# Optimization experiments

Hardware: AMD Instinct MI355X
Metric: run time of the kernel (lower is better)

Reference implementation:

```python
import jax, jax.numpy as jnp
import numpy as np

HEADS = 4

def _dwconv(x, w, pad):
    # depthwise conv, NCHW, kernel [C,1,k,k]
    return jax.lax.conv_general_dilated(
        x, w, window_strides=(1, 1), padding=((pad, pad), (pad, pad)),
        feature_group_count=x.shape[1],
        dimension_numbers=('NCHW', 'OIHW', 'NCHW'))

def _l2norm(t):
    # matches torch F.normalize(dim=-1, eps=1e-12)
    n = jnp.sqrt(jnp.sum(t * t, axis=-1, keepdims=True))
    return t / jnp.maximum(n, 1e-12)

def _reshape_attn(q, k, v, temp, if_box):
    b, c, hw0 = q.shape
    factor = HEADS
    ch = c // HEADS
    pad = (-hw0) % factor

    def prep(t):
        t = jnp.pad(t, ((0, 0), (0, 0), (0, pad)))
        hw = t.shape[-1] // factor
        if if_box:  # 'b (head c) (factor hw) -> b head (c factor) hw'
            t = t.reshape(b, HEADS, ch, factor, hw)
        else:       # 'b (head c) (hw factor) -> b head (c factor) hw'
            t = t.reshape(b, HEADS, ch, hw, factor).transpose(0, 1, 2, 4, 3)
        return t.reshape(b, HEADS, ch * factor, hw)

    qq, kk, vv = prep(q), prep(k), prep(v)
    qq, kk = _l2norm(qq), _l2norm(kk)
    attn = jnp.einsum('bhdn,bhen->bhde', qq, kk) * temp  # temp [heads,1,1]
    e = jnp.exp(attn)
    attn = e / (jnp.sum(e, axis=-1, keepdims=True) + 1.0)  # softmax_1
    o = jnp.einsum('bhde,bhen->bhdn', attn, vv)
    hw = o.shape[-1]
    if if_box:
        o = o.reshape(b, HEADS, ch, factor, hw).reshape(b, c, factor * hw)
    else:
        o = o.reshape(b, HEADS, ch, factor, hw).transpose(0, 1, 2, 4, 3).reshape(b, c, hw * factor)
    return o[:, :, :hw0]

def _conv1x1(x, w):
    return jnp.einsum('bchw,oc->bohw', x, w)

def _forward(x, temperature, w_qkv, w_dw3, w_dw5, w_dw7, w_fuse, b_fuse, w_proj):
    b, c, h, w = x.shape
    ch = c // 2
    # sort first half of channels along h then w
    xh = x[:, :ch]
    idx_h = jnp.argsort(xh, axis=-2)
    xs = jnp.take_along_axis(xh, idx_h, axis=-2)
    idx_w = jnp.argsort(xs, axis=-1)
    xs = jnp.take_along_axis(xs, idx_w, axis=-1)
    x = jnp.concatenate([xs, x[:, ch:]], axis=1)

    q = _conv1x1(x, w_qkv)  # [b,5c,h,w]
    cat = jnp.concatenate([_dwconv(q, w_dw3, 1), _dwconv(q, w_dw5, 2), _dwconv(q, w_dw7, 3)], axis=1)
    qkv = _conv1x1(cat, w_fuse) + b_fuse[None, :, None, None]
    q1, k1, q2, k2, v = jnp.split(qkv, 5, axis=1)

    hw = h * w
    vf = v.reshape(b, c, hw)
    idx = jnp.argsort(vf, axis=-1)
    vs = jnp.take_along_axis(vf, idx, axis=-1)
    gat = lambda t: jnp.take_along_axis(t.reshape(b, c, hw), idx, axis=-1)

    out1 = _reshape_attn(gat(q1), gat(k1), vs, temperature, True)
    out2 = _reshape_attn(gat(q2), gat(k2), vs, temperature, False)

    inv = jnp.argsort(idx, axis=-1)  # scatter(out, 2, idx, out) == unsort
    out1 = jnp.take_along_axis(out1, inv, axis=-1).reshape(b, c, h, w)
    out2 = jnp.take_along_axis(out2, inv, axis=-1).reshape(b, c, h, w)

    out = _conv1x1(out1 * out2, w_proj)
    r = out[:, :ch]
    r = jnp.take_along_axis(r, jnp.argsort(idx_w, axis=-1), axis=-1)
    r = jnp.take_along_axis(r, jnp.argsort(idx_h, axis=-2), axis=-2)
    return jnp.concatenate([r, out[:, ch:]], axis=1)

def setup_inputs() -> dict:
    key = jax.random.key(0)
    ks = jax.random.split(key, 8)
    b, c, h, w = 2, 64, 192, 192
    x = jax.random.normal(ks[0], (b, c, h, w), jnp.float32)
    temperature = jnp.ones((HEADS, 1, 1), jnp.float32)
    w_qkv = jax.random.normal(ks[1], (5 * c, c), jnp.float32) * 0.05
    w_dw3 = jax.random.normal(ks[2], (5 * c, 1, 3, 3), jnp.float32) * 0.1
    w_dw5 = jax.random.normal(ks[3], (5 * c, 1, 5, 5), jnp.float32) * 0.05
    w_dw7 = jax.random.normal(ks[4], (5 * c, 1, 7, 7), jnp.float32) * 0.03
    w_fuse = jax.random.normal(ks[5], (5 * c, 15 * c), jnp.float32) * 0.02
    b_fuse = jnp.zeros((5 * c,), jnp.float32)
    w_proj = jax.random.normal(ks[6], (c, c), jnp.float32) * 0.05
    return {'x': x, 'temperature': temperature, 'w_qkv': w_qkv, 'w_dw3': w_dw3,
            'w_dw5': w_dw5, 'w_dw7': w_dw7, 'w_fuse': w_fuse, 'b_fuse': b_fuse,
            'w_proj': w_proj}

def reference(x, temperature, w_qkv, w_dw3, w_dw5, w_dw7, w_fuse, b_fuse, w_proj):
    return _forward(x, temperature, w_qkv, w_dw3, w_dw5, w_dw7, w_fuse, b_fuse, w_proj)
```

## Files before the change

kernel.cpp:

```cpp
#include <hip/hip_runtime.h>
#include <stdint.h>
#include <stddef.h>

constexpr int IMH = 192;
constexpr int IMW = 192;
constexpr int HW  = 36864;
constexpr int BB  = 2;
constexpr int CC  = 64;
constexpr int CHF = 32;
constexpr int C5  = 320;
constexpr int NQ  = 9216;
constexpr int CROWS = 64;
constexpr int CHWN  = CROWS * IMW;
constexpr int NCHUNK = 32;
constexpr int CHN = HW / 4 / NCHUNK;
constexpr int NSEG = 16;
constexpr int SEGN = HW / NSEG;
constexpr int NBIN = 2048;

typedef float fx4 __attribute__((ext_vector_type(4)));
typedef _Float16 f16;
typedef _Float16 f16x8 __attribute__((ext_vector_type(8)));
typedef float f32x4 __attribute__((ext_vector_type(4)));

static __device__ __forceinline__ uint32_t f2s(float f) {
    uint32_t u = __float_as_uint(f);
    return (u & 0x80000000u) ? ~u : (u | 0x80000000u);
}
static __device__ __forceinline__ float s2f(uint32_t s) {
    uint32_t u = (s & 0x80000000u) ? (s & 0x7FFFFFFFu) : ~s;
    return __uint_as_float(u);
}

static __device__ void bitonic256(uint64_t* keys, int tid) {
    for (unsigned k = 2; k <= 256; k <<= 1) {
        for (unsigned j = k >> 1; j; j >>= 1) {
            __syncthreads();
            unsigned i = ((tid & ~(j - 1)) << 1) | (tid & (j - 1));
            unsigned p = i | j;
            bool up = ((i & k) == 0);
            uint64_t a = keys[i], b = keys[p];
            if ((a > b) == up) { keys[i] = b; keys[p] = a; }
        }
    }
    __syncthreads();
}

__global__ void k_copy_back(const float* __restrict__ x, float* __restrict__ A) {
    int i = blockIdx.x * 256 + threadIdx.x;
    int b = i / (CHF * HW);
    int r = i % (CHF * HW);
    size_t o = ((size_t)(b * CC) + CHF) * HW + r;
    A[o] = x[o];
}

__global__ __launch_bounds__(128) void k_sort_h(const float* __restrict__ x, float* __restrict__ A,
                                                int* __restrict__ idx_h) {
    __shared__ uint64_t keys[256];
    int tid = threadIdx.x;
    int blk = blockIdx.x;
    int w = blk % IMW;
    int c = (blk / IMW) % CHF;
    int b = blk / (IMW * CHF);
    const float* col = x + ((size_t)(b * CC) + c) * HW + w;
    for (int i = tid; i < 256; i += 128)
        keys[i] = (i < IMH) ? ((((uint64_t)f2s(col[(size_t)i * IMW])) << 32) | (uint32_t)i) : ~0ull;
    bitonic256(keys, tid);
    float* ocol = A + ((size_t)(b * CC) + c) * HW + w;
    int* icol = idx_h + ((size_t)(b * CHF) + c) * HW + w;
    for (int i = tid; i < IMH; i += 128) {
        uint64_t k = keys[i];
        ocol[(size_t)i * IMW] = s2f((uint32_t)(k >> 32));
        icol[(size_t)i * IMW] = (int)(k & 0xFFFFFFFFull);
    }
}

__global__ __launch_bounds__(128) void k_sort_w(float* __restrict__ A, int* __restrict__ idx_w) {
    __shared__ uint64_t keys[256];
    int tid = threadIdx.x;
    int blk = blockIdx.x;
    int h = blk % IMH;
    int c = (blk / IMH) % CHF;
    int b = blk / (IMH * CHF);
    float* row = A + ((size_t)(b * CC) + c) * HW + (size_t)h * IMW;
    for (int i = tid; i < 256; i += 128)
        keys[i] = (i < IMW) ? ((((uint64_t)f2s(row[i])) << 32) | (uint32_t)i) : ~0ull;
    bitonic256(keys, tid);
    int* irow = idx_w + ((size_t)(b * CHF) + c) * HW + (size_t)h * IMW;
    for (int i = tid; i < IMW; i += 128) {
        uint64_t k = keys[i];
        row[i] = s2f((uint32_t)(k >> 32));
        irow[i] = (int)(k & 0xFFFFFFFFull);
    }
}

__global__ __launch_bounds__(256) void k_gemm_q(const float* __restrict__ wq, const float* __restrict__ A,
                                                float* __restrict__ q) {
    __shared__ float Wt[64][68];
    __shared__ float Xt[64][68];
    int tid = threadIdx.x;
    int n0 = blockIdx.x * 64, m0 = blockIdx.y * 64, b = blockIdx.z;
    for (int l = 0; l < 16; ++l) {
        int idx = l * 256 + tid;
        int cc = idx & 63, m = idx >> 6;
        Wt[cc][m] = wq[(size_t)(m0 + m) * 64 + cc];
    }
    for (int l = 0; l < 16; ++l) {
        int idx = l * 256 + tid;
        int n = idx & 63, cc = idx >> 6;
        Xt[cc][n] = A[((size_t)(b * CC) + cc) * HW + n0 + n];
    }
    __syncthreads();
    int ty = tid >> 4, tx = tid & 15;
    float acc[4][4] = {};
    for (int cc = 0; cc < 64; ++cc) {
        float4 av = *(const float4*)&Wt[cc][ty * 4];
        float4 bv = *(const float4*)&Xt[cc][tx * 4];
        float aa[4] = {av.x, av.y, av.z, av.w};
        float bb[4] = {bv.x, bv.y, bv.z, bv.w};
        #pragma unroll
        for (int i = 0; i < 4; ++i)
            #pragma unroll
            for (int j = 0; j < 4; ++j)
                acc[i][j] = fmaf(aa[i], bb[j], acc[i][j]);
    }
    for (int i = 0; i < 4; ++i) {
        float4 o;
        o.x = acc[i][0]; o.y = acc[i][1]; o.z = acc[i][2]; o.w = acc[i][3];
        *(float4*)&q[((size_t)(b * C5) + m0 + ty * 4 + i) * HW + n0 + tx * 4] = o;
    }
}

template <int KS>
__global__ __launch_bounds__(256) void k_dwconv(const float* __restrict__ q, const float* __restrict__ wd,
                                                float* __restrict__ slice, int r0) {
    constexpr int PAD = KS / 2;
    constexpr int EXT = 32 + 2 * PAD;
    __shared__ float tile[EXT][EXT];
    int tid = threadIdx.x;
    int b = blockIdx.z, c = blockIdx.y;
    int t = blockIdx.x;
    int ty0 = r0 + (t / 6) * 32, tx0 = (t % 6) * 32;
    const float* src = q + ((size_t)(b * C5) + c) * HW;
    for (int i = tid; i < EXT * EXT; i += 256) {
        int iy = i / EXT, ix = i % EXT;
        int gy = ty0 + iy - PAD, gx = tx0 + ix - PAD;
        float v = 0.f;
        if (gy >= 0 && gy < IMH && gx >= 0 && gx < IMW) v = src[gy * IMW + gx];
        tile[iy][ix] = v;
    }
    __syncthreads();
    float wreg[KS * KS];
    #pragma unroll
    for (int i = 0; i < KS * KS; ++i) wreg[i] = wd[(size_t)c * KS * KS + i];
    float* dst = slice + ((size_t)(b * C5) + c) * CHWN;
    #pragma unroll
    for (int k = 0; k < 4; ++k) {
        int pix = k * 256 + tid;
        int py = pix >> 5, px = pix & 31;
        float acc = 0.f;
        #pragma unroll
        for (int ky = 0; ky < KS; ++ky)
            #pragma unroll
            for (int kx = 0; kx < KS; ++kx)
                acc = fmaf(tile[py + ky][px + kx], wreg[ky * KS + kx], acc);
        dst[(ty0 - r0 + py) * IMW + tx0 + px] = acc;
    }
}

__global__ __launch_bounds__(256) void k_gemm_fuse(const float* __restrict__ wf,
                                                   const float* __restrict__ slice, const float* __restrict__ bias,
                                                   float* __restrict__ qkv, int g, int r0) {
    __shared__ f16 Ah[64][40];
    __shared__ f16 Al[64][40];
    int tid = threadIdx.x;
    int n0 = blockIdx.x * 128, m0 = blockIdx.y * 64, b = blockIdx.z;
    int lane = tid & 63, wv = tid >> 6;
    int l15 = lane & 15, lg = lane >> 4;
    int nwave = n0 + wv * 32;
    int sm = tid >> 2, skr = (tid & 3) * 8;
    int gk = g * 320;
    f32x4 acc[4][2];
    #pragma unroll
    for (int i = 0; i < 4; ++i)
        #pragma unroll
        for (int j = 0; j < 2; ++j)
            acc[i][j] = (f32x4){0.f, 0.f, 0.f, 0.f};

    const float* xcol = slice + (size_t)(b * C5) * CHWN + nwave + l15;
    const float* wrow = wf + (size_t)(m0 + sm) * 960 + gk + skr;

    for (int k0 = 0; k0 < 320; k0 += 32) {
        if (k0) __syncthreads();
        {
            float4 w0 = *(const float4*)(wrow + k0);
            float4 w1 = *(const float4*)(wrow + k0 + 4);
            float wvv[8] = {w0.x, w0.y, w0.z, w0.w, w1.x, w1.y, w1.z, w1.w};
            f16x8 hv, lv;
            #pragma unroll
            for (int j = 0; j < 8; ++j) {
                f16 h = (f16)wvv[j];
                hv[j] = h;
                lv[j] = (f16)(wvv[j] - (float)h);
            }
            *(f16x8*)&Ah[sm][skr] = hv;
            *(f16x8*)&Al[sm][skr] = lv;
        }
        float xv[2][8];
        #pragma unroll
        for (int fn = 0; fn < 2; ++fn)
            #pragma unroll
            for (int j = 0; j < 8; ++j)
                xv[fn][j] = xcol[(size_t)(k0 + lg * 8 + j) * CHWN + fn * 16];
        __syncthreads();
        f16x8 bh[2], bl[2];
        #pragma unroll
        for (int fn = 0; fn < 2; ++fn)
            #pragma unroll
            for (int j = 0; j < 8; ++j) {
                float v = xv[fn][j];
                f16 h = (f16)v;
                bh[fn][j] = h;
                bl[fn][j] = (f16)(v - (float)h);
            }
        #pragma unroll
        for (int fm = 0; fm < 4; ++fm) {
            f16x8 ah = *(const f16x8*)&Ah[fm * 16 + l15][lg * 8];
            f16x8 al = *(const f16x8*)&Al[fm * 16 + l15][lg * 8];
            #pragma unroll
            for (int fn = 0; fn < 2; ++fn) {
                acc[fm][fn] = __builtin_amdgcn_mfma_f32_16x16x32_f16(ah, bh[fn], acc[fm][fn], 0, 0, 0);
                acc[fm][fn] = __builtin_amdgcn_mfma_f32_16x16x32_f16(ah, bl[fn], acc[fm][fn], 0, 0, 0);
                acc[fm][fn] = __builtin_amdgcn_mfma_f32_16x16x32_f16(al, bh[fn], acc[fm][fn], 0, 0, 0);
            }
        }
    }

    #pragma unroll
    for (int fm = 0; fm < 4; ++fm) {
        #pragma unroll
        for (int r = 0; r < 4; ++r) {
            int m = m0 + fm * 16 + lg * 4 + r;
            size_t base = ((size_t)(b * C5) + m) * HW + (size_t)r0 * IMW;
            if (g == 0) {
                float bv = bias[m];
                #pragma unroll
                for (int fn = 0; fn < 2; ++fn)
                    qkv[base + nwave + fn * 16 + l15] = acc[fm][fn][r] + bv;
            } else {
                #pragma unroll
                for (int fn = 0; fn < 2; ++fn)
                    qkv[base + nwave + fn * 16 + l15] += acc[fm][fn][r];
            }
        }
    }
}

__global__ void k_build_keys(const float* __restrict__ qkv, uint64_t* __restrict__ keyA) {
    int j = blockIdx.x * 256 + threadIdx.x;
    int row = blockIdx.y;
    int b = row >> 6, c = row & 63;
    float v = qkv[((size_t)(b * C5) + 256 + c) * HW + j];
    keyA[(size_t)row * HW + j] = (((uint64_t)f2s(v)) << 32) | (uint32_t)j;
}

__global__ __launch_bounds__(256) void k_rcount(const uint64_t* __restrict__ in, uint32_t* __restrict__ cntG,
                                                int shift) {
    __shared__ uint32_t hist[NBIN];
    int t = threadIdx.x;
    int seg = blockIdx.x, row = blockIdx.y;
    #pragma unroll
    for (int k = 0; k < NBIN / 256; ++k) hist[k * 256 + t] = 0;
    __syncthreads();
    const uint64_t* src = in + (size_t)row * HW + (size_t)seg * SEGN;
    #pragma unroll
    for (int i = 0; i < SEGN / 256; ++i) {
        unsigned d = (unsigned)(src[i * 256 + t] >> shift) & (NBIN - 1);
        atomicAdd(&hist[d], 1u);
    }
    __syncthreads();
    uint32_t* dstc = cntG + ((size_t)row * NSEG + seg) * NBIN;
    #pragma unroll
    for (int k = 0; k < NBIN / 256; ++k) dstc[k * 256 + t] = hist[k * 256 + t];
}

__global__ __launch_bounds__(256) void k_rscan(uint32_t* __restrict__ cntG) {
    __shared__ uint32_t tot[NBIN];
    __shared__ uint32_t gsum[256];
    __shared__ uint32_t gbase[256];
    int t = threadIdx.x;
    int row = blockIdx.x;
    uint32_t* base = cntG + (size_t)row * NSEG * NBIN;
    uint32_t loc = 0;
    #pragma unroll
    for (int k = 0; k < NBIN / 256; ++k) {
        int bn = t * (NBIN / 256) + k;
        uint32_t s = 0;
        for (int sg = 0; sg < NSEG; ++sg) s += base[sg * NBIN + bn];
        tot[bn] = s;
        loc += s;
    }
    gsum[t] = loc;
    __syncthreads();
    if (t == 0) {
        uint32_t acc = 0;
        for (int i = 0; i < 256; ++i) { uint32_t v = gsum[i]; gbase[i] = acc; acc += v; }
    }
    __syncthreads();
    uint32_t run = gbase[t];
    #pragma unroll
    for (int k = 0; k < NBIN / 256; ++k) {
        int bn = t * (NBIN / 256) + k;
        uint32_t tv = tot[bn];
        uint32_t r2 = run;
        for (int sg = 0; sg < NSEG; ++sg) {
            uint32_t cv = base[sg * NBIN + bn];
            base[sg * NBIN + bn] = r2;
            r2 += cv;
        }
        run += tv;
    }
}

__global__ __launch_bounds__(256) void k_rscatter(const uint64_t* __restrict__ in, uint64_t* __restrict__ out,
                                                  const uint32_t* __restrict__ cntG, int shift) {
    __shared__ uint16_t wcnt[4][NBIN];
    __shared__ uint32_t runbase[NBIN];
    int t = threadIdx.x;
    int w = t >> 6, lane = t & 63;
    int seg = blockIdx.x, row = blockIdx.y;
    const uint32_t* cbase = cntG + ((size_t)row * NSEG + seg) * NBIN;
    #pragma unroll
    for (int k = 0; k < NBIN / 256; ++k) runbase[k * 256 + t] = cbase[k * 256 + t];
    const uint64_t* src = in + (size_t)row * HW + (size_t)seg * SEGN;
    uint64_t* dst = out + (size_t)row * HW;
    for (int i = 0; i < SEGN / 256; ++i) {
        __syncthreads();
        #pragma unroll
        for (int k = 0; k < NBIN / 256; ++k)
            ((uint64_t*)wcnt)[k * 256 + t] = 0;
        __syncthreads();
        uint64_t kv = src[i * 256 + t];
        unsigned d = (unsigned)(kv >> shift) & (NBIN - 1);
        uint64_t peers = ~0ull;
        #pragma unroll
        for (int bit = 0; bit < 11; ++bit) {
            uint64_t bm = __ballot((d >> bit) & 1u);
            peers &= ((d >> bit) & 1u) ? bm : ~bm;
        }
        unsigned lanerank = (unsigned)__popcll(peers & ((1ull << lane) - 1ull));
        unsigned wtotal = (unsigned)__popcll(peers);
        if (lanerank == 0) wcnt[w][d] = (uint16_t)wtotal;
        __syncthreads();
        unsigned wpre = 0;
        #pragma unroll
        for (int ww = 0; ww < 4; ++ww) {
            unsigned cv = wcnt[ww][d];
            if (ww < w) wpre += cv;
        }
        unsigned pos = runbase[d] + wpre + lanerank;
        dst[pos] = kv;
        __syncthreads();
        #pragma unroll
        for (int k = 0; k < NBIN / 256; ++k) {
            int bn = k * 256 + t;
            runbase[bn] += (uint32_t)wcnt[0][bn] + wcnt[1][bn] + wcnt[2][bn] + wcnt[3][bn];
        }
    }
}

__global__ void k_unpack(const uint64_t* __restrict__ keys, float* __restrict__ vs, int* __restrict__ idxv) {
    int j = blockIdx.x * 256 + threadIdx.x;
    int row = blockIdx.y;
    size_t o = (size_t)row * HW + j;
    uint64_t k = keys[o];
    vs[o] = s2f((uint32_t)(k >> 32));
    idxv[o] = (int)(k & 0xFFFFFFFFull);
}

__global__ __launch_bounds__(1024) void k_gather4(const int* __restrict__ idxv, const float* __restrict__ qkv,
                                                  float* __restrict__ g4) {
    int i = blockIdx.x;
    int row = (i & 7) * 16 + ((i >> 3) & 15);
    int jh = i >> 7;
    int b = row >> 6, cg = row & 63;
    const int* irow = idxv + (size_t)row * HW + jh * (HW / 2);
    size_t S4 = (size_t)BB * CC * HW;
    int tid = threadIdx.x;
    for (int ph = 0; ph < 4; ++ph) {
        const float* src = qkv + ((size_t)(b * C5) + ph * 64 + cg) * HW;
        float* dst = g4 + (size_t)ph * S4 + (size_t)row * HW + jh * (HW / 2);
        #pragma unroll 2
        for (int j = tid; j < HW / 2; j += 1024)
            dst[j] = src[irow[j]];
        __syncthreads();
    }
}

__global__ __launch_bounds__(256) void k_attn_qk(const float* __restrict__ g4,
                                                 float* __restrict__ partS, float* __restrict__ partN) {
    __shared__ float Qs[16][68];
    __shared__ float Ks[16][68];
    __shared__ float nqs[4][64];
    __shared__ float nks[4][64];
    int tid = threadIdx.x;
    int ychunk = blockIdx.x;
    int z = blockIdx.y;
    int vi = z & 1, hh = (z >> 1) & 3, b = z >> 3;
    size_t S4 = (size_t)BB * CC * HW;
    const float* Q = g4 + (vi ? 2 * S4 : (size_t)0);
    const float* Kp = g4 + (vi ? 3 * S4 : S4);
    int ty = tid >> 4, tx = tid & 15;
    float acc[4][4] = {};
    float nq = 0.f, nk = 0.f;
    int d0 = tid & 63, kset = tid >> 6;
    int nbase0 = ychunk * CHN;
    for (int it = 0; it < CHN / 16; ++it) {
        int nb0 = nbase0 + it * 16;
        __syncthreads();
        #pragma unroll
        for (int l = 0; l < 4; ++l) {
            int idx = l * 256 + tid;
            int d = idx >> 4, kk = idx & 15;
            int n = nb0 + kk;
            int cch = hh * 16 + (d >> 2), f = d & 3;
            size_t off = ((size_t)(b * CC) + cch) * HW + (vi ? (size_t)(n * 4 + f) : (size_t)(f * NQ + n));
            Qs[kk][d] = Q[off];
            Ks[kk][d] = Kp[off];
        }
        __syncthreads();
        #pragma unroll
        for (int kk = 0; kk < 16; ++kk) {
            float4 av = *(const float4*)&Qs[kk][ty * 4];
            float4 bv = *(const float4*)&Ks[kk][tx * 4];
            float aa[4] = {av.x, av.y, av.z, av.w};
            float bb[4] = {bv.x, bv.y, bv.z, bv.w};
            #pragma unroll
            for (int i = 0; i < 4; ++i)
                #pragma unroll
                for (int j = 0; j < 4; ++j)
                    acc[i][j] = fmaf(aa[i], bb[j], acc[i][j]);
        }
        #pragma unroll
        for (int kk2 = 0; kk2 < 4; ++kk2) {
            float qv = Qs[kset * 4 + kk2][d0];
            float kv = Ks[kset * 4 + kk2][d0];
            nq = fmaf(qv, qv, nq);
            nk = fmaf(kv, kv, nk);
        }
    }
    size_t sb = ((size_t)z * NCHUNK + ychunk) * 4096;
    #pragma unroll
    for (int i = 0; i < 4; ++i)
        #pragma unroll
        for (int j = 0; j < 4; ++j)
            partS[sb + (size_t)(ty * 4 + i) * 64 + tx * 4 + j] = acc[i][j];
    nqs[kset][d0] = nq;
    nks[kset][d0] = nk;
    __syncthreads();
    if (tid < 64) {
        float sq = nqs[0][tid] + nqs[1][tid] + nqs[2][tid] + nqs[3][tid];
        float sk = nks[0][tid] + nks[1][tid] + nks[2][tid] + nks[3][tid];
        size_t nb2 = ((size_t)z * NCHUNK + ychunk) * 128;
        partN[nb2 + tid] = sq;
        partN[nb2 + 64 + tid] = sk;
    }
}

__global__ __launch_bounds__(256) void k_attn_softmax(const float* __restrict__ partS,
                                                      const float* __restrict__ partN,
                                                      const float* __restrict__ temp, float* __restrict__ attnT) {
    __shared__ float nqv[64], nkv[64];
    __shared__ float pbuf[64][65];
    __shared__ float rred[64][4];
    __shared__ float rsum[64];
    int tid = threadIdx.x;
    int z = blockIdx.x;
    int hh = (z >> 1) & 3;
    if (tid < 128) {
        float s = 0.f;
        for (int ch = 0; ch < NCHUNK; ++ch) s += partN[((size_t)z * NCHUNK + ch) * 128 + tid];
        float nv = fmaxf(sqrtf(s), 1e-12f);
        if (tid < 64) nqv[tid] = nv; else nkv[tid - 64] = nv;
    }
    __syncthreads();
    float tf = temp[hh];
    int d = tid >> 2, qq = tid & 3;
    float psum = 0.f;
    for (int e = qq * 16; e < qq * 16 + 16; ++e) {
        float s = 0.f;
        for (int ch = 0; ch < NCHUNK; ++ch) s += partS[((size_t)z * NCHUNK + ch) * 4096 + (size_t)d * 64 + e];
        float p = expf(tf * s / (nqv[d] * nkv[e]));
        pbuf[d][e] = p;
        psum += p;
    }
    rred[d][qq] = psum;
    __syncthreads();
    if (tid < 64) rsum[tid] = rred[tid][0] + rred[tid][1] + rred[tid][2] + rred[tid][3] + 1.0f;
    __syncthreads();
    for (int e = qq * 16; e < qq * 16 + 16; ++e)
        attnT[(size_t)z * 4096 + (size_t)e * 64 + d] = pbuf[d][e] / rsum[d];
}

__global__ __launch_bounds__(256) void k_attn_av(const float* __restrict__ attnT, const float* __restrict__ vs,
                                                 float* __restrict__ O1, float* __restrict__ O2) {
    __shared__ float at_s[4096];
    int tid = threadIdx.x;
    int z = blockIdx.y;
    int vi = z & 1, hh = (z >> 1) & 3, b = z >> 3;
    for (int l = 0; l < 16; ++l) at_s[l * 256 + tid] = attnT[(size_t)z * 4096 + l * 256 + tid];
    __syncthreads();
    int n = blockIdx.x * 256 + tid;
    float acc[64];
    #pragma unroll
    for (int d = 0; d < 64; ++d) acc[d] = 0.f;
    for (int e = 0; e < 64; ++e) {
        int cch = hh * 16 + (e >> 2), f = e & 3;
        size_t p = vi ? (size_t)(n * 4 + f) : (size_t)(f * NQ + n);
        float vv = vs[((size_t)(b * CC) + cch) * HW + p];
        const float* ar = &at_s[e * 64];
        #pragma unroll
        for (int d4 = 0; d4 < 16; ++d4) {
            float4 a4 = *(const float4*)&ar[d4 * 4];
            acc[d4 * 4 + 0] = fmaf(a4.x, vv, acc[d4 * 4 + 0]);
            acc[d4 * 4 + 1] = fmaf(a4.y, vv, acc[d4 * 4 + 1]);
            acc[d4 * 4 + 2] = fmaf(a4.z, vv, acc[d4 * 4 + 2]);
            acc[d4 * 4 + 3] = fmaf(a4.w, vv, acc[d4 * 4 + 3]);
        }
    }
    float* Ob = vi ? O2 : O1;
    #pragma unroll
    for (int d = 0; d < 64; ++d) {
        int cch = hh * 16 + (d >> 2), f = d & 3;
        size_t p = vi ? (size_t)(n * 4 + f) : (size_t)(f * NQ + n);
        Ob[((size_t)(b * CC) + cch) * HW + p] = acc[d];
    }
}

__global__ void k_prod_scatter(const float* __restrict__ O1, const float* __restrict__ O2,
                               const int* __restrict__ idxv, float* __restrict__ pu) {
    int j = blockIdx.x * 256 + threadIdx.x;
    int row = blockIdx.y;
    size_t o = (size_t)row * HW + j;
    int p = idxv[o];
    pu[(size_t)row * HW + p] = O1[o] * O2[o];
}

__global__ __launch_bounds__(256) void k_gemm_proj(const float* __restrict__ wp, const float* __restrict__ pu,
                                                   float* __restrict__ op) {
    __shared__ float wt[4096];
    int tid = threadIdx.x;
    for (int l = 0; l < 16; ++l) {
        int i = l * 256 + tid;
        int m = i >> 6, c = i & 63;
        wt[c * 64 + m] = wp[i];
    }
    __syncthreads();
    int b = blockIdx.y;
    int n = blockIdx.x * 256 + tid;
    float acc[64];
    #pragma unroll
    for (int m = 0; m < 64; ++m) acc[m] = 0.f;
    const float* src = pu + (size_t)(b * CC) * HW + n;
    for (int c = 0; c < 64; ++c) {
        float xv = src[(size_t)c * HW];
        const float* wr = &wt[c * 64];
        #pragma unroll
        for (int m4 = 0; m4 < 16; ++m4) {
            float4 w4 = *(const float4*)&wr[m4 * 4];
            acc[m4 * 4 + 0] = fmaf(w4.x, xv, acc[m4 * 4 + 0]);
            acc[m4 * 4 + 1] = fmaf(w4.y, xv, acc[m4 * 4 + 1]);
            acc[m4 * 4 + 2] = fmaf(w4.z, xv, acc[m4 * 4 + 2]);
            acc[m4 * 4 + 3] = fmaf(w4.w, xv, acc[m4 * 4 + 3]);
        }
    }
    float* dst = op + (size_t)(b * CC) * HW + n;
    for (int m = 0; m < 64; ++m) dst[(size_t)m * HW] = acc[m];
}

__global__ void k_final(const float* __restrict__ op, const int* __restrict__ idx_h,
                        const int* __restrict__ idx_w, float* __restrict__ out) {
    int i = blockIdx.x * 256 + threadIdx.x;
    int p = i % HW;
    int c = (i / HW) % CC;
    int b = i / (HW * CC);
    float v = op[i];
    if (c < CHF) {
        int h = p / IMW, w = p % IMW;
        size_t ib = ((size_t)(b * CHF) + c) * HW;
        int W0 = idx_w[ib + h * IMW + w];
        int H0 = idx_h[ib + h * IMW + W0];
        out[((size_t)(b * CC) + c) * HW + H0 * IMW + W0] = v;
    } else {
        out[i] = v;
    }
}

extern "C" void kernel_launch(void* const* d_in, const int* in_sizes, int n_in,
                              void* d_out, int out_size, void* d_ws, size_t ws_size,
                              hipStream_t stream) {
    (void)in_sizes; (void)n_in; (void)out_size; (void)ws_size;
    const float* x    = (const float*)d_in[0];
    const float* temp = (const float*)d_in[1];
    const float* wq   = (const float*)d_in[2];
    const float* wd3  = (const float*)d_in[3];
    const float* wd5  = (const float*)d_in[4];
    const float* wd7  = (const float*)d_in[5];
    const float* wf   = (const float*)d_in[6];
    const float* bf   = (const float*)d_in[7];
    const float* wp   = (const float*)d_in[8];
    float* out = (float*)d_out;
    float* ws = (float*)d_ws;

    int*      idx_h = (int*)(ws + 0);
    int*      idx_w = (int*)(ws + 2359296);
    float*    A     = ws + 4718592;
    float*    slice = ws + 4718592;
    float*    q     = ws + 12582912;
    float*    qkv   = ws + 36175872;
    uint64_t* keyA  = (uint64_t*)(ws + 12582912);
    uint64_t* keyB  = (uint64_t*)(ws + 22020096);
    float*    vs    = ws + 31457280;
    uint32_t* cntG  = (uint32_t*)(ws + 4718592);
    int*      idxv  = (int*)(ws + 4718592);
    float*    g4    = ws + 12582912;
    float*    O1    = ws + 36175872;
    float*    O2    = ws + 40894464;
    float*    pu    = ws + 45613056;
    float*    op    = ws + 50331648;
    float*    partS = ws + 55050240;
    float*    partN = ws + 57147392;
    float*    attnT = ws + 57212928;

    k_copy_back<<<9216, 256, 0, stream>>>(x, A);
    k_sort_h<<<12288, 128, 0, stream>>>(x, A, idx_h);
    k_sort_w<<<12288, 128, 0, stream>>>(A, idx_w);
    k_gemm_q<<<dim3(576, 5, 2), 256, 0, stream>>>(wq, A, q);

    for (int g = 0; g < 3; ++g) {
        for (int chunk = 0; chunk < 3; ++chunk) {
            int r0 = chunk * CROWS;
            if (g == 0)      k_dwconv<3><<<dim3(12, 320, 2), 256, 0, stream>>>(q, wd3, slice, r0);
            else if (g == 1) k_dwconv<5><<<dim3(12, 320, 2), 256, 0, stream>>>(q, wd5, slice, r0);
            else             k_dwconv<7><<<dim3(12, 320, 2), 256, 0, stream>>>(q, wd7, slice, r0);
            k_gemm_fuse<<<dim3(96, 5, 2), 256, 0, stream>>>(wf, slice, bf, qkv, g, r0);
        }
    }

    k_build_keys<<<dim3(144, 128), 256, 0, stream>>>(qkv, keyA);
    const int shifts[3] = {32, 43, 54};
    for (int p = 0; p < 3; ++p) {
        const uint64_t* src = (p & 1) ? keyB : keyA;
        uint64_t*       dst = (p & 1) ? keyA : keyB;
        k_rcount  <<<dim3(NSEG, 128), 256, 0, stream>>>(src, cntG, shifts[p]);
        k_rscan   <<<128, 256, 0, stream>>>(cntG);
        k_rscatter<<<dim3(NSEG, 128), 256, 0, stream>>>(src, dst, cntG, shifts[p]);
    }
    k_unpack<<<dim3(144, 128), 256, 0, stream>>>(keyB, vs, idxv);
    k_gather4<<<256, 1024, 0, stream>>>(idxv, qkv, g4);

    k_attn_qk<<<dim3(NCHUNK, 16), 256, 0, stream>>>(g4, partS, partN);
    k_attn_softmax<<<16, 256, 0, stream>>>(partS, partN, temp, attnT);
    k_attn_av<<<dim3(36, 16), 256, 0, stream>>>(attnT, vs, O1, O2);

    k_prod_scatter<<<dim3(144, 128), 256, 0, stream>>>(O1, O2, idxv, pu);
    k_gemm_proj<<<dim3(144, 2), 256, 0, stream>>>(wp, pu, op);
    k_final<<<18432, 256, 0, stream>>>(op, idx_h, idx_w, out);
}
```

Before: 1.236 ms.

## Fuse key build and unpack into radix passes, drop copy-back, vectorize gather

The first radix count and scatter passes now build keys straight from qkv, and the last scatter pass writes the sorted values and indices directly. This removes the separate build-keys and unpack kernels and their extra round trips through global memory. The copy-back kernel is dropped: the q GEMM reads unsorted channels directly from x. The gather now preloads its indices into registers and uses non-temporal paired stores, NSEG drops from 16 to 12, and the workspace offsets for cntG and idxv are moved so the buffers do not overlap.

```diff
diff --git a/kernel.cpp b/kernel.cpp
--- a/kernel.cpp
+++ b/kernel.cpp
@@ -14,10 +14,11 @@
 constexpr int CHWN  = CROWS * IMW;
 constexpr int NCHUNK = 32;
 constexpr int CHN = HW / 4 / NCHUNK;
-constexpr int NSEG = 16;
+constexpr int NSEG = 12;
 constexpr int SEGN = HW / NSEG;
 constexpr int NBIN = 2048;
 
+typedef float fx2 __attribute__((ext_vector_type(2)));
 typedef float fx4 __attribute__((ext_vector_type(4)));
 typedef _Float16 f16;
 typedef _Float16 f16x8 __attribute__((ext_vector_type(8)));
@@ -44,14 +45,6 @@
         }
     }
     __syncthreads();
-}
-
-__global__ void k_copy_back(const float* __restrict__ x, float* __restrict__ A) {
-    int i = blockIdx.x * 256 + threadIdx.x;
-    int b = i / (CHF * HW);
-    int r = i % (CHF * HW);
-    size_t o = ((size_t)(b * CC) + CHF) * HW + r;
-    A[o] = x[o];
 }
 
 __global__ __launch_bounds__(128) void k_sort_h(const float* __restrict__ x, float* __restrict__ A,
@@ -95,7 +88,7 @@
 }
 
 __global__ __launch_bounds__(256) void k_gemm_q(const float* __restrict__ wq, const float* __restrict__ A,
-                                                float* __restrict__ q) {
+                                                const float* __restrict__ x, float* __restrict__ q) {
     __shared__ float Wt[64][68];
     __shared__ float Xt[64][68];
     int tid = threadIdx.x;
@@ -108,7 +101,8 @@
     for (int l = 0; l < 16; ++l) {
         int idx = l * 256 + tid;
         int n = idx & 63, cc = idx >> 6;
-        Xt[cc][n] = A[((size_t)(b * CC) + cc) * HW + n0 + n];
+        const float* sp = (cc < CHF) ? A : x;
+        Xt[cc][n] = sp[((size_t)(b * CC) + cc) * HW + n0 + n];
     }
     __syncthreads();
     int ty = tid >> 4, tx = tid & 15;
@@ -256,27 +250,30 @@
     }
 }
 
-__global__ void k_build_keys(const float* __restrict__ qkv, uint64_t* __restrict__ keyA) {
-    int j = blockIdx.x * 256 + threadIdx.x;
-    int row = blockIdx.y;
-    int b = row >> 6, c = row & 63;
-    float v = qkv[((size_t)(b * C5) + 256 + c) * HW + j];
-    keyA[(size_t)row * HW + j] = (((uint64_t)f2s(v)) << 32) | (uint32_t)j;
-}
-
-__global__ __launch_bounds__(256) void k_rcount(const uint64_t* __restrict__ in, uint32_t* __restrict__ cntG,
-                                                int shift) {
+template <int FIRST>
+__global__ __launch_bounds__(256) void k_rcount(const uint64_t* __restrict__ in, const float* __restrict__ qkvv,
+                                                uint32_t* __restrict__ cntG, int shift) {
     __shared__ uint32_t hist[NBIN];
     int t = threadIdx.x;
     int seg = blockIdx.x, row = blockIdx.y;
     #pragma unroll
     for (int k = 0; k < NBIN / 256; ++k) hist[k * 256 + t] = 0;
     __syncthreads();
-    const uint64_t* src = in + (size_t)row * HW + (size_t)seg * SEGN;
-    #pragma unroll
-    for (int i = 0; i < SEGN / 256; ++i) {
-        unsigned d = (unsigned)(src[i * 256 + t] >> shift) & (NBIN - 1);
-        atomicAdd(&hist[d], 1u);
+    if (FIRST) {
+        int bb = row >> 6, c = row & 63;
+        const float* srcf = qkvv + ((size_t)(bb * C5) + 256 + c) * HW + (size_t)seg * SEGN;
+        #pragma unroll
+        for (int i = 0; i < SEGN / 256; ++i) {
+            unsigned d = f2s(srcf[i * 256 + t]) & (NBIN - 1);
+            atomicAdd(&hist[d], 1u);
+        }
+    } else {
+        const uint64_t* src = in + (size_t)row * HW + (size_t)seg * SEGN;
+        #pragma unroll
+        for (int i = 0; i < SEGN / 256; ++i) {
+            unsigned d = (unsigned)(src[i * 256 + t] >> shift) & (NBIN - 1);
+            atomicAdd(&hist[d], 1u);
+        }
     }
     __syncthreads();
     uint32_t* dstc = cntG + ((size_t)row * NSEG + seg) * NBIN;
@@ -322,8 +319,11 @@
     }
 }
 
-__global__ __launch_bounds__(256) void k_rscatter(const uint64_t* __restrict__ in, uint64_t* __restrict__ out,
-                                                  const uint32_t* __restrict__ cntG, int shift) {
+template <int MODE>
+__global__ __launch_bounds__(256) void k_rscatter(const uint64_t* __restrict__ in, const float* __restrict__ qkvv,
+                                                  uint64_t* __restrict__ out, float* __restrict__ vso,
+                                                  int* __restrict__ idxo, const uint32_t* __restrict__ cntG,
+                                                  int shift) {
     __shared__ uint16_t wcnt[4][NBIN];
     __shared__ uint32_t runbase[NBIN];
     int t = threadIdx.x;
@@ -332,15 +332,21 @@
     const uint32_t* cbase = cntG + ((size_t)row * NSEG + seg) * NBIN;
     #pragma unroll
     for (int k = 0; k < NBIN / 256; ++k) runbase[k * 256 + t] = cbase[k * 256 + t];
-    const uint64_t* src = in + (size_t)row * HW + (size_t)seg * SEGN;
-    uint64_t* dst = out + (size_t)row * HW;
     for (int i = 0; i < SEGN / 256; ++i) {
         __syncthreads();
         #pragma unroll
         for (int k = 0; k < NBIN / 256; ++k)
             ((uint64_t*)wcnt)[k * 256 + t] = 0;
         __syncthreads();
-        uint64_t kv = src[i * 256 + t];
+        uint64_t kv;
+        if (MODE == 1) {
+            int bb = row >> 6, c = row & 63;
+            const float* srcf = qkvv + ((size_t)(bb * C5) + 256 + c) * HW + (size_t)seg * SEGN;
+            kv = (((uint64_t)f2s(srcf[i * 256 + t])) << 32) | (uint32_t)(seg * SEGN + i * 256 + t);
+        } else {
+            const uint64_t* src = in + (size_t)row * HW + (size_t)seg * SEGN;
+            kv = src[i * 256 + t];
+        }
         unsigned d = (unsigned)(kv >> shift) & (NBIN - 1);
         uint64_t peers = ~0ull;
         #pragma unroll
@@ -359,7 +365,12 @@
             if (ww < w) wpre += cv;
         }
         unsigned pos = runbase[d] + wpre + lanerank;
-        dst[pos] = kv;
+        if (MODE == 2) {
+            vso[(size_t)row * HW + pos] = s2f((uint32_t)(kv >> 32));
+            idxo[(size_t)row * HW + pos] = (int)(kv & 0xFFFFFFFFull);
+        } else {
+            out[(size_t)row * HW + pos] = kv;
+        }
         __syncthreads();
         #pragma unroll
         for (int k = 0; k < NBIN / 256; ++k) {
@@ -367,15 +378,6 @@
             runbase[bn] += (uint32_t)wcnt[0][bn] + wcnt[1][bn] + wcnt[2][bn] + wcnt[3][bn];
         }
     }
-}
-
-__global__ void k_unpack(const uint64_t* __restrict__ keys, float* __restrict__ vs, int* __restrict__ idxv) {
-    int j = blockIdx.x * 256 + threadIdx.x;
-    int row = blockIdx.y;
-    size_t o = (size_t)row * HW + j;
-    uint64_t k = keys[o];
-    vs[o] = s2f((uint32_t)(k >> 32));
-    idxv[o] = (int)(k & 0xFFFFFFFFull);
 }
 
 __global__ __launch_bounds__(1024) void k_gather4(const int* __restrict__ idxv, const float* __restrict__ qkv,
@@ -387,12 +389,20 @@
     const int* irow = idxv + (size_t)row * HW + jh * (HW / 2);
     size_t S4 = (size_t)BB * CC * HW;
     int tid = threadIdx.x;
+    int2 pidx[9];
+    #pragma unroll
+    for (int s = 0; s < 9; ++s)
+        pidx[s] = *(const int2*)&irow[s * 2048 + tid * 2];
     for (int ph = 0; ph < 4; ++ph) {
         const float* src = qkv + ((size_t)(b * C5) + ph * 64 + cg) * HW;
         float* dst = g4 + (size_t)ph * S4 + (size_t)row * HW + jh * (HW / 2);
-        #pragma unroll 2
-        for (int j = tid; j < HW / 2; j += 1024)
-            dst[j] = src[irow[j]];
+        #pragma unroll 3
+        for (int s = 0; s < 9; ++s) {
+            fx2 v;
+            v.x = src[pidx[s].x];
+            v.y = src[pidx[s].y];
+            __builtin_nontemporal_store(v, (fx2*)&dst[s * 2048 + tid * 2]);
+        }
         __syncthreads();
     }
 }
@@ -618,11 +628,11 @@
     float*    slice = ws + 4718592;
     float*    q     = ws + 12582912;
     float*    qkv   = ws + 36175872;
+    int*      idxv  = (int*)(ws + 4718592);
+    uint32_t* cntG  = (uint32_t*)(ws + 9437184);
     uint64_t* keyA  = (uint64_t*)(ws + 12582912);
     uint64_t* keyB  = (uint64_t*)(ws + 22020096);
     float*    vs    = ws + 31457280;
-    uint32_t* cntG  = (uint32_t*)(ws + 4718592);
-    int*      idxv  = (int*)(ws + 4718592);
     float*    g4    = ws + 12582912;
     float*    O1    = ws + 36175872;
     float*    O2    = ws + 40894464;
@@ -632,10 +642,9 @@
     float*    partN = ws + 57147392;
     float*    attnT = ws + 57212928;
 
-    k_copy_back<<<9216, 256, 0, stream>>>(x, A);
     k_sort_h<<<12288, 128, 0, stream>>>(x, A, idx_h);
     k_sort_w<<<12288, 128, 0, stream>>>(A, idx_w);
-    k_gemm_q<<<dim3(576, 5, 2), 256, 0, stream>>>(wq, A, q);
+    k_gemm_q<<<dim3(576, 5, 2), 256, 0, stream>>>(wq, A, x, q);
 
     for (int g = 0; g < 3; ++g) {
         for (int chunk = 0; chunk < 3; ++chunk) {
@@ -647,16 +656,16 @@
         }
     }
 
-    k_build_keys<<<dim3(144, 128), 256, 0, stream>>>(qkv, keyA);
-    const int shifts[3] = {32, 43, 54};
-    for (int p = 0; p < 3; ++p) {
-        const uint64_t* src = (p & 1) ? keyB : keyA;
-        uint64_t*       dst = (p & 1) ? keyA : keyB;
-        k_rcount  <<<dim3(NSEG, 128), 256, 0, stream>>>(src, cntG, shifts[p]);
-        k_rscan   <<<128, 256, 0, stream>>>(cntG);
-        k_rscatter<<<dim3(NSEG, 128), 256, 0, stream>>>(src, dst, cntG, shifts[p]);
-    }
-    k_unpack<<<dim3(144, 128), 256, 0, stream>>>(keyB, vs, idxv);
+    k_rcount<1><<<dim3(NSEG, 128), 256, 0, stream>>>(nullptr, qkv, cntG, 32);
+    k_rscan<<<128, 256, 0, stream>>>(cntG);
+    k_rscatter<1><<<dim3(NSEG, 128), 256, 0, stream>>>(nullptr, qkv, keyB, nullptr, nullptr, cntG, 32);
+    k_rcount<0><<<dim3(NSEG, 128), 256, 0, stream>>>(keyB, nullptr, cntG, 43);
+    k_rscan<<<128, 256, 0, stream>>>(cntG);
+    k_rscatter<0><<<dim3(NSEG, 128), 256, 0, stream>>>(keyB, nullptr, keyA, nullptr, nullptr, cntG, 43);
+    k_rcount<0><<<dim3(NSEG, 128), 256, 0, stream>>>(keyA, nullptr, cntG, 54);
+    k_rscan<<<128, 256, 0, stream>>>(cntG);
+    k_rscatter<2><<<dim3(NSEG, 128), 256, 0, stream>>>(keyA, nullptr, nullptr, vs, idxv, cntG, 54);
+
     k_gather4<<<256, 1024, 0, stream>>>(idxv, qkv, g4);
 
     k_attn_qk<<<dim3(NCHUNK, 16), 256, 0, stream>>>(g4, partS, partN);
```

Measured after the change: 1.217 ms. About the same (-1.5%).
